# Kernel tuning notes

Measured on AMD Instinct MI355X. Metric: run time of the kernel, lower is better.

Reference implementation:

```python
import jax, jax.numpy as jnp
import numpy as np

H = 2048
MAX_DEPTH = 2
BASIS = 4


def setup_inputs() -> dict:
    key = jax.random.key(0)
    ks = jax.random.split(key, 16)
    s = 0.02

    def w(k, shape):
        return jax.random.normal(k, shape, dtype=jnp.float32) * s

    return dict(
        x=jax.random.normal(ks[0], (1, H), dtype=jnp.float32),
        h=jax.random.normal(ks[1], (1, H), dtype=jnp.float32),
        c=jax.random.normal(ks[2], (1, H), dtype=jnp.float32),
        Wq=w(ks[3], (H, H)), Wk=w(ks[4], (H, H)), Wv=w(ks[5], (H, H)), Wo=w(ks[6], (H, H)),
        Wih=w(ks[7], (H, 4 * H)), Whh=w(ks[8], (H, 4 * H)),
        b_lstm=jnp.zeros((4 * H,), jnp.float32),
        router_w=w(ks[9], (H, BASIS)), router_b=jnp.zeros((BASIS,), jnp.float32),
        expert_w=w(ks[10], (BASIS, H, H)), expert_b=jnp.zeros((BASIS, H), jnp.float32),
        dr_w=w(ks[11], (H, MAX_DEPTH + 1)),
        # bias the depth router toward the deepest choice so the recursion tree is exercised
        dr_b=jnp.array([0.0, 1.0, 5.0], jnp.float32),
        ram_w=w(ks[12], (2 * H, H)), ram_b=jnp.zeros((H,), jnp.float32),
        ag_w=w(ks[13], (2 * H, H)), ag_b=jnp.zeros((H,), jnp.float32),
    )


def reference(x, h, c, Wq, Wk, Wv, Wo, Wih, Whh, b_lstm, router_w, router_b,
              expert_w, expert_b, dr_w, dr_b, ram_w, ram_b, ag_w, ag_b):
    def cell_step(x_, h_, c_):
        # Single-token multi-head attention: softmax over a length-1 axis is
        # identically 1, so attention collapses to (h @ Wv) @ Wo; Wq/Wk are
        # parameters with zero effective gradient (matches torch behavior).
        attn = (h_ @ Wv) @ Wo
        gates = x_ @ Wih + attn @ Whh + b_lstm  # [1, 4H]
        i, f, g, o = jnp.split(gates, 4, axis=1)
        c2 = jax.nn.sigmoid(f) * c_ + jax.nn.sigmoid(i) * jnp.tanh(g)
        h2 = jax.nn.sigmoid(o) * jnp.tanh(c2)
        return h2, h2, c2

    def path_gate(hh):
        p = jax.nn.softmax(hh @ router_w + router_b, axis=1)          # [1, E]
        eo = jnp.einsum('bh,ehk->bek', hh, expert_w) + expert_b        # [1, E, H]
        return jnp.einsum('be,bek->bk', p, eo)                         # [1, H]

    def ramanujan(states):
        # alternating-harmonic (Ramanujan-summation style) weighted reduction
        agg = states[0] * 0.0
        for n, s in enumerate(states):
            agg = agg + (((-1.0) ** n) / (n + 1)) * s
        return jnp.concatenate([agg, states[0]], axis=1) @ ram_w + ram_b

    def fwd(x_, h_, c_, depth):
        so, hs, cs = cell_step(x_, h_, c_)
        hp = path_gate(hs)
        # mirrors torch.no_grad() + .item() host sync
        chosen = int(jnp.argmax(hp @ dr_w + dr_b, axis=1)[0])
        steps = min(chosen, max(0, MAX_DEPTH - depth))
        if steps <= 0:
            return so, hp, cs
        h_cur, c_cur, final = hp, cs, so
        states = [h_cur]
        for _ in range(steps):
            damping = 1.0 / (depth + 1) ** 2
            ro, hnr, cn = fwd(x_, h_cur, c_cur, depth + 1)
            h_next = h_cur + damping * (hnr - h_cur)  # torch.lerp
            states.append(h_next)
            h_cur, c_cur, final = h_next, cn, ro
        anchor = ramanujan(states)
        g = jax.nn.sigmoid(jnp.concatenate([h_cur, anchor], axis=1) @ ag_w + ag_b)
        return final, g * anchor + (1.0 - g) * h_cur, c_cur

    return fwd(x, h, c, 0)
```

## Files before the change

### kernel.cpp

```cpp
#include <hip/hip_runtime.h>
#include <math.h>


#define H 2048
#define NB 512
#define PREP_NB 2048
typedef unsigned short u16;
typedef float f4v __attribute__((ext_vector_type(4)));

struct P {
  const float *x, *h0, *c0, *Wv, *Wo, *Wih, *Whh, *b_lstm, *router_w, *router_b,
              *expert_w, *expert_b, *dr_w, *dr_b, *ram_w, *ram_b, *ag_w, *ag_b;
  const u16 *bWv, *bWo, *bWhh, *bEx, *bRam, *bAg;
  float* out;
  float* ws;
};

constexpr int CTRU   = 16384;
constexpr int DL     = 16384;
constexpr int GT     = 16400;
constexpr int NODE   = 24592;
constexpr int NODESZ = 26624;
constexpr int THV = 0, ATT = 2048, GAC = 4096, EO = 12288, SO = 20480, CS = 22528, HP = 24576;
constexpr int FIN    = NODE + 5 * NODESZ;
constexpr int FINSZ  = 8192;
constexpr int ANC = 0, GCC = 2048, HNo = 4096, AGGo = 6144;
constexpr int RH1 = FIN + 3 * FINSZ;
constexpr int RF1 = RH1 + 2048;
constexpr int RC1 = RH1 + 4096;
constexpr int ZTOT = 5 * 20480 + 3 * 4096;
constexpr size_t BF_BYTE_OFF = 786432;
constexpr size_t oWo  = 4194304;
constexpr size_t oWhh = 8388608;
constexpr size_t oEx  = 25165824;
constexpr size_t oRam = 41943040;
constexpr size_t oAg  = 50331648;
constexpr size_t BF_NODE = 41943040;
constexpr size_t BF_ALL  = 58720256;

__device__ __forceinline__ float sigm(float v) { return 1.f / (1.f + expf(-v)); }

__device__ __forceinline__ float coh_f(const float* p) {
  return __hip_atomic_load(p, __ATOMIC_RELAXED, __HIP_MEMORY_SCOPE_AGENT);
}
__device__ __forceinline__ void coh_st(float* p, float v) {
  __hip_atomic_store(p, v, __ATOMIC_RELAXED, __HIP_MEMORY_SCOPE_AGENT);
}

__device__ __forceinline__ float bfl(unsigned u) { union { unsigned x; float f; } c; c.x = u << 16; return c.f; }
__device__ __forceinline__ float bfh(unsigned u) { union { unsigned x; float f; } c; c.x = u & 0xFFFF0000u; return c.f; }
__device__ __forceinline__ u16 f2bf(float f) {
  unsigned u = __float_as_uint(f);
  u += 0x7FFFu + ((u >> 16) & 1u);
  return (u16)(u >> 16);
}

template <typename WT> struct W4;
template <> struct W4<float> {
  static __device__ __forceinline__ void load(const float* p, float* w) {
    const float4 v = *reinterpret_cast<const float4*>(p);
    w[0] = v.x; w[1] = v.y; w[2] = v.z; w[3] = v.w;
  }
};
template <> struct W4<u16> {
  static __device__ __forceinline__ void load(const u16* p, float* w) {
    const uint2 u = *reinterpret_cast<const uint2*>(p);
    w[0] = bfl(u.x); w[1] = bfh(u.x); w[2] = bfl(u.y); w[3] = bfh(u.y);
  }
};

template <typename WT> __device__ __forceinline__ const WT* selWv(const P& p);
template <> __device__ __forceinline__ const float* selWv<float>(const P& p) { return p.Wv; }
template <> __device__ __forceinline__ const u16*   selWv<u16>(const P& p)   { return p.bWv; }
template <typename WT> __device__ __forceinline__ const WT* selWo(const P& p);
template <> __device__ __forceinline__ const float* selWo<float>(const P& p) { return p.Wo; }
template <> __device__ __forceinline__ const u16*   selWo<u16>(const P& p)   { return p.bWo; }
template <typename WT> __device__ __forceinline__ const WT* selWhh(const P& p);
template <> __device__ __forceinline__ const float* selWhh<float>(const P& p) { return p.Whh; }
template <> __device__ __forceinline__ const u16*   selWhh<u16>(const P& p)   { return p.bWhh; }
template <typename WT> __device__ __forceinline__ const WT* selEx(const P& p);
template <> __device__ __forceinline__ const float* selEx<float>(const P& p) { return p.expert_w; }
template <> __device__ __forceinline__ const u16*   selEx<u16>(const P& p)   { return p.bEx; }
template <typename WT> __device__ __forceinline__ const WT* selRam(const P& p);
template <> __device__ __forceinline__ const float* selRam<float>(const P& p) { return p.ram_w; }
template <> __device__ __forceinline__ const u16*   selRam<u16>(const P& p)   { return p.bRam; }
template <typename WT> __device__ __forceinline__ const WT* selAg(const P& p);
template <> __device__ __forceinline__ const float* selAg<float>(const P& p) { return p.ag_w; }
template <> __device__ __forceinline__ const u16*   selAg<u16>(const P& p)   { return p.bAg; }

__device__ __forceinline__ int dsteps(const float* dla, const float* drb, int mx) {
  const float l0 = coh_f(dla + 0) + drb[0];
  const float l1 = coh_f(dla + 1) + drb[1];
  const float l2 = coh_f(dla + 2) + drb[2];
  int ch = 0; float bv = l0;
  if (l1 > bv) { bv = l1; ch = 1; }
  if (l2 > bv) { bv = l2; ch = 2; }
  return ch < mx ? ch : mx;
}

__device__ __forceinline__ bool pred(const float* ws, const float* drb, int code) {
  if (code == 0) return true;
  const int s0 = dsteps(ws + DL, drb, 2);
  switch (code) {
    case 1: return s0 >= 1;
    case 2: return s0 >= 1 && dsteps(ws + DL + 4, drb, 1) >= 1;
    case 3: return s0 >= 2;
    case 4: return s0 >= 2 && dsteps(ws + DL + 8, drb, 1) >= 1;
  }
  return true;
}

__device__ __forceinline__ void resbar(unsigned* ctr, int phase) {
  asm volatile("s_waitcnt vmcnt(0)" ::: "memory");
  __syncthreads();
  __shared__ int lastB;
  if (threadIdx.x == 0) {
    lastB = 0;
    unsigned* line = ctr + (blockIdx.x & 31) * 16;
    const unsigned prev = __hip_atomic_fetch_add(line, 1u, __ATOMIC_RELAXED, __HIP_MEMORY_SCOPE_AGENT);
    if (prev == (unsigned)(16 * phase) - 1u) {
      const unsigned m = __hip_atomic_fetch_add(ctr + 512, 1u, __ATOMIC_RELAXED, __HIP_MEMORY_SCOPE_AGENT);
      if (m == (unsigned)(32 * phase) - 1u) lastB = 1;
    }
  }
  __syncthreads();
  if (lastB) {
    if (threadIdx.x < 32)
      __hip_atomic_store(ctr + (40 + threadIdx.x) * 16, (unsigned)phase,
                         __ATOMIC_RELAXED, __HIP_MEMORY_SCOPE_AGENT);
  } else if (threadIdx.x == 0) {
    const unsigned* rel = ctr + (40 + (blockIdx.x & 31)) * 16;
    long t = 0;
    while (__hip_atomic_load(rel, __ATOMIC_RELAXED, __HIP_MEMORY_SCOPE_AGENT) < (unsigned)phase) {
      __builtin_amdgcn_s_sleep(2);
      if (++t > 30000000L) break;
    }
  }
  __syncthreads();
}

template <int CHUNK, int XMODE, typename WT>
__device__ __forceinline__ void gemv_phase(
    int bid, int G,
    const float* xA, const float* xB, int splitPt, const float* xBias,
    const WT* __restrict__ W, float* __restrict__ y, int N,
    float* shx, float4* red)
{
  const int tid = threadIdx.x, lane = tid & 63, tsub = tid >> 6;
  const int g = bid % G, s = bid / G;
  const int base = s * CHUNK;
  for (int idx = tid; idx < CHUNK; idx += 256) {
    const int i = base + idx;
    float v;
    if (XMODE == 0)      v = (i < splitPt) ? xA[i] : xB[i - splitPt];
    else if (XMODE == 1) v = coh_f(xA + i);
    else                 v = (i < splitPt) ? xA[i] : (xBias[i - splitPt] + coh_f(xB + (i - splitPt)));
    shx[idx] = v;
  }
  __syncthreads();
  constexpr int LEN = CHUNK / 4;
  const int j = (g << 8) + (lane << 2);
  const WT* Wp = W + (size_t)(base + tsub * LEN) * N + j;
  float ax = 0.f, ay = 0.f, az = 0.f, aw = 0.f;
#pragma unroll
  for (int t = 0; t < LEN; ++t) {
    const float xi = shx[tsub * LEN + t];
    float w[4];
    W4<WT>::load(Wp + (size_t)t * N, w);
    ax = fmaf(xi, w[0], ax); ay = fmaf(xi, w[1], ay);
    az = fmaf(xi, w[2], az); aw = fmaf(xi, w[3], aw);
  }
  red[tid] = make_float4(ax, ay, az, aw);
  __syncthreads();
  if (tsub == 0) {
    float4 a = red[tid], b = red[tid + 64], c = red[tid + 128], d = red[tid + 192];
    atomicAdd(&y[j + 0], a.x + b.x + c.x + d.x);
    atomicAdd(&y[j + 1], a.y + b.y + c.y + d.y);
    atomicAdd(&y[j + 2], a.z + b.z + c.z + d.z);
    atomicAdd(&y[j + 3], a.w + b.w + c.w + d.w);
  }
}

template <typename WT>
__device__ void expert_phase(const P& p, float* nb, const float* c_in, const float* gt,
                             float* shx, float4* red)
{
  const int tid = threadIdx.x, lane = tid & 63, w = tid >> 6;
  const int g = blockIdx.x & 31, s = blockIdx.x >> 5;
  const int i0 = s * 128;
  if (tid < 128) {
    const int i = i0 + tid;
    const float gi = p.b_lstm[i]         + coh_f(gt + i)         + coh_f(nb + GAC + i);
    const float gf = p.b_lstm[H + i]     + coh_f(gt + H + i)     + coh_f(nb + GAC + H + i);
    const float gg = p.b_lstm[2 * H + i] + coh_f(gt + 2 * H + i) + coh_f(nb + GAC + 2 * H + i);
    const float go = p.b_lstm[3 * H + i] + coh_f(gt + 3 * H + i) + coh_f(nb + GAC + 3 * H + i);
    const float c2 = sigm(gf) * c_in[i] + sigm(gi) * tanhf(gg);
    const float h2 = sigm(go) * tanhf(c2);
    shx[tid] = h2;
    if (g == 0) { coh_st(nb + SO + i, h2); coh_st(nb + CS + i, c2); }
  }
  __syncthreads();
  const int j = (g << 8) + (lane << 2);
  const int e = j >> 11, k = j & (H - 1);
  const WT* Wp = selEx<WT>(p) + ((size_t)e << 22) + (size_t)(i0 + w * 32) * H + k;
  float ax = 0.f, ay = 0.f, az = 0.f, aw = 0.f;
#pragma unroll
  for (int t = 0; t < 32; ++t) {
    const float xi = shx[w * 32 + t];
    float wv[4];
    W4<WT>::load(Wp + (size_t)t * H, wv);
    ax = fmaf(xi, wv[0], ax); ay = fmaf(xi, wv[1], ay);
    az = fmaf(xi, wv[2], az); aw = fmaf(xi, wv[3], aw);
  }
  red[tid] = make_float4(ax, ay, az, aw);
  __syncthreads();
  if (w == 0) {
    float4 a = red[tid], b = red[tid + 64], c = red[tid + 128], d = red[tid + 192];
    atomicAdd(&nb[EO + j + 0], a.x + b.x + c.x + d.x);
    atomicAdd(&nb[EO + j + 1], a.y + b.y + c.y + d.y);
    atomicAdd(&nb[EO + j + 2], a.z + b.z + c.z + d.z);
    atomicAdd(&nb[EO + j + 3], a.w + b.w + c.w + d.w);
  }
}

__device__ void combine_phase(const P& p, float* nb, float* dla, int leaf, float damping,
                              const float* php, float* hn, float* agg, float4* red)
{
  const int tid = threadIdx.x;
  float r0 = 0.f, r1 = 0.f, r2 = 0.f, r3 = 0.f;
  for (int i = tid; i < H; i += 256) {
    const float hh = coh_f(nb + SO + i);
    const float4 rw = *reinterpret_cast<const float4*>(p.router_w + i * 4);
    r0 = fmaf(hh, rw.x, r0); r1 = fmaf(hh, rw.y, r1);
    r2 = fmaf(hh, rw.z, r2); r3 = fmaf(hh, rw.w, r3);
  }
  red[tid] = make_float4(r0, r1, r2, r3);
  __syncthreads();
  for (int off = 128; off > 0; off >>= 1) {
    if (tid < off) {
      const float4 b = red[tid + off];
      red[tid].x += b.x; red[tid].y += b.y; red[tid].z += b.z; red[tid].w += b.w;
    }
    __syncthreads();
  }
  const float4 L = red[0];
  __syncthreads();
  const float l0 = L.x + p.router_b[0], l1 = L.y + p.router_b[1];
  const float l2 = L.z + p.router_b[2], l3 = L.w + p.router_b[3];
  const float m = fmaxf(fmaxf(l0, l1), fmaxf(l2, l3));
  const float e0 = expf(l0 - m), e1 = expf(l1 - m), e2 = expf(l2 - m), e3 = expf(l3 - m);
  const float inv = 1.f / (e0 + e1 + e2 + e3);
  const float q0 = e0 * inv, q1 = e1 * inv, q2 = e2 * inv, q3 = e3 * inv;
  const int jj = blockIdx.x * 256 + tid;
  const float v = q0 * (p.expert_b[jj]         + coh_f(nb + EO + jj))
                + q1 * (p.expert_b[H + jj]     + coh_f(nb + EO + H + jj))
                + q2 * (p.expert_b[2 * H + jj] + coh_f(nb + EO + 2 * H + jj))
                + q3 * (p.expert_b[3 * H + jj] + coh_f(nb + EO + 3 * H + jj));
  if (leaf) {
    const float h0v = php[jj];
    const float hnv = h0v + damping * (v - h0v);
    hn[jj] = hnv;
    agg[jj] = h0v - 0.5f * hnv;
  } else {
    nb[HP + jj] = v;
    red[tid] = make_float4(v * p.dr_w[jj * 3 + 0], v * p.dr_w[jj * 3 + 1], v * p.dr_w[jj * 3 + 2], 0.f);
    __syncthreads();
    for (int off = 128; off > 0; off >>= 1) {
      if (tid < off) {
        const float4 b = red[tid + off];
        red[tid].x += b.x; red[tid].y += b.y; red[tid].z += b.z;
      }
      __syncthreads();
    }
    if (tid == 0) {
      atomicAdd(&dla[0], red[0].x);
      atomicAdd(&dla[1], red[0].y);
      atomicAdd(&dla[2], red[0].z);
    }
  }
}

__device__ void tail_fsel(const P& p, float* ws) {
  if (dsteps(ws + DL, p.dr_b, 2) < 1) return;
  const bool deep = dsteps(ws + DL + 4, p.dr_b, 1) >= 1;
  const int jj = blockIdx.x * 256 + threadIdx.x;
  const float* n1 = ws + NODE + 1 * NODESZ;
  const float* n2 = ws + NODE + 2 * NODESZ;
  const float* fb = ws + FIN;
  float rh, rf, rc;
  if (deep) {
    const float gacc = p.ag_b[jj] + coh_f(fb + GCC + jj);
    const float anc  = p.ram_b[jj] + coh_f(fb + ANC + jj);
    const float g = sigm(gacc);
    rh = g * anc + (1.f - g) * fb[HNo + jj];
    rf = n2[SO + jj]; rc = n2[CS + jj];
  } else {
    rh = n1[HP + jj]; rf = n1[SO + jj]; rc = n1[CS + jj];
  }
  ws[RH1 + jj] = rh; ws[RF1 + jj] = rf; ws[RC1 + jj] = rc;
}

__device__ void tail1(const P& p, float* ws) {
  const int s0 = dsteps(ws + DL, p.dr_b, 2);
  if (s0 < 1) return;
  const int jj = blockIdx.x * 256 + threadIdx.x;
  const float* n0 = ws + NODE;
  const float* n3 = ws + NODE + 3 * NODESZ;
  const float* n4 = ws + NODE + 4 * NODESZ;
  const float* fb3 = ws + FIN + FINSZ;
  float* fb0 = ws + FIN + 2 * FINSZ;
  const float r1 = ws[RH1 + jj];
  float rh3 = 0.f, rf3 = 0.f, rc3 = 0.f;
  if (s0 >= 2) {
    if (dsteps(ws + DL + 8, p.dr_b, 1) >= 1) {
      const float gacc = p.ag_b[jj] + coh_f(fb3 + GCC + jj);
      const float anc  = p.ram_b[jj] + coh_f(fb3 + ANC + jj);
      const float g = sigm(gacc);
      rh3 = g * anc + (1.f - g) * fb3[HNo + jj];
      rf3 = n4[SO + jj]; rc3 = n4[CS + jj];
    } else { rh3 = n3[HP + jj]; rf3 = n3[SO + jj]; rc3 = n3[CS + jj]; }
  }
  float ag = n0[HP + jj] - 0.5f * r1;
  float hc, oF, oC;
  if (s0 >= 2) { ag += (1.f / 3.f) * rh3; hc = rh3; oF = rf3; oC = rc3; }
  else { hc = r1; oF = ws[RF1 + jj]; oC = ws[RC1 + jj]; }
  fb0[AGGo + jj] = ag; fb0[HNo + jj] = hc;
  p.out[jj] = oF; p.out[2 * H + jj] = oC;
}

__device__ void tail2(const P& p, float* ws) {
  const int s0 = dsteps(ws + DL, p.dr_b, 2);
  const int jj = blockIdx.x * 256 + threadIdx.x;
  const float* n0 = ws + NODE;
  const float* fb0 = ws + FIN + 2 * FINSZ;
  if (s0 == 0) {
    p.out[jj] = n0[SO + jj]; p.out[H + jj] = n0[HP + jj]; p.out[2 * H + jj] = n0[CS + jj];
  } else {
    const float gacc = p.ag_b[jj] + coh_f(fb0 + GCC + jj);
    const float anc  = p.ram_b[jj] + coh_f(fb0 + ANC + jj);
    const float g = sigm(gacc);
    p.out[H + jj] = g * anc + (1.f - g) * fb0[HNo + jj];
  }
}

__global__ void __launch_bounds__(256) k_zero(P p) {
  float* ws = p.ws;
  const int gtid = blockIdx.x * 256 + threadIdx.x;
  const int gsz = gridDim.x * 256;
  unsigned* u = (unsigned*)ws;
  for (int i = gtid; i < CTRU; i += gsz) u[i] = 0u;
  if (gtid < 12) ws[DL + gtid] = 0.f;
  for (int i = gtid; i < 8192; i += gsz) ws[GT + i] = 0.f;
}

__global__ void __launch_bounds__(256) k_prep(P p, u16* bf, int convMask) {
  float* ws = p.ws;
  __shared__ float shx[128];
  __shared__ float4 red[256];
  const size_t gtid = (size_t)blockIdx.x * 256 + threadIdx.x;
  const size_t nthr = (size_t)PREP_NB * 256;
  for (size_t i = gtid; i < (size_t)ZTOT; i += nthr) {
    if (i < 5 * 20480) {
      const int n = (int)(i / 20480), off = (int)(i % 20480);
      ws[NODE + n * NODESZ + off] = 0.f;
    } else {
      const int j = (int)(i - 5 * 20480);
      ws[FIN + (j >> 12) * FINSZ + (j & 4095)] = 0.f;
    }
  }
  auto conv = [&](const float* __restrict__ src, u16* __restrict__ dst, size_t elems) {
    for (size_t c = gtid; c < elems / 8; c += nthr) {
      const size_t e = c * 8;
      const f4v a = __builtin_nontemporal_load(reinterpret_cast<const f4v*>(src + e));
      const f4v b = __builtin_nontemporal_load(reinterpret_cast<const f4v*>(src + e + 4));
      uint4 o;
      o.x = (unsigned)f2bf(a.x) | ((unsigned)f2bf(a.y) << 16);
      o.y = (unsigned)f2bf(a.z) | ((unsigned)f2bf(a.w) << 16);
      o.z = (unsigned)f2bf(b.x) | ((unsigned)f2bf(b.y) << 16);
      o.w = (unsigned)f2bf(b.z) | ((unsigned)f2bf(b.w) << 16);
      *reinterpret_cast<uint4*>(dst + e) = o;
    }
  };
  if (convMask & 1) {
    conv(p.Wv,       bf,         oWo);
    conv(p.Wo,       bf + oWo,   oWhh - oWo);
    conv(p.Whh,      bf + oWhh,  oEx - oWhh);
    conv(p.expert_w, bf + oEx,   oRam - oEx);
  }
  if (convMask & 2) {
    conv(p.ram_w, bf + oRam, oAg - oRam);
    conv(p.ag_w,  bf + oAg,  BF_ALL - oAg);
  }
  gemv_phase<32, 0, float>(blockIdx.x, 32, p.x, p.x, 1 << 30, nullptr,
                           p.Wih, ws + GT, 4 * H, shx, red);
}

template <typename WT>
__global__ void __launch_bounds__(256, 2) k_node(
    P p, int nodeIdx, int ctrIdx, int predCode,
    const float* hv, const float* cv,
    int leaf, float damping, const float* php, float* hn, float* agg, float* dla)
{
  float* ws = p.ws;
  if (!pred(ws, p.dr_b, predCode)) return;
  __shared__ float shx[128];
  __shared__ float4 red[256];
  float* nb = ws + NODE + nodeIdx * NODESZ;
  unsigned* ctr = (unsigned*)ws + ctrIdx * 2048;
  gemv_phase<32, 0, WT>(blockIdx.x, 8, hv, hv, 1 << 30, nullptr, selWv<WT>(p), nb + THV, H, shx, red);
  resbar(ctr, 1);
  gemv_phase<32, 1, WT>(blockIdx.x, 8, nb + THV, nullptr, 0, nullptr, selWo<WT>(p), nb + ATT, H, shx, red);
  resbar(ctr, 2);
  gemv_phase<128, 1, WT>(blockIdx.x, 32, nb + ATT, nullptr, 0, nullptr, selWhh<WT>(p), nb + GAC, 4 * H, shx, red);
  resbar(ctr, 3);
  expert_phase<WT>(p, nb, cv, ws + GT, shx, red);
  resbar(ctr, 4);
  if (blockIdx.x >= 8) return;
  combine_phase(p, nb, dla, leaf, damping, php, hn, agg, red);
}

template <typename WT>
__global__ void __launch_bounds__(256, 2) k_fin(
    P p, int finIdx, int ctrIdx, int predCode,
    const float* aggv, const float* phpv, const float* hnv, int tailKind)
{
  float* ws = p.ws;
  __shared__ float shx[64];
  __shared__ float4 red[256];
  float* fb = ws + FIN + finIdx * FINSZ;
  unsigned* ctr = (unsigned*)ws + ctrIdx * 2048;
  const bool ok = pred(ws, p.dr_b, predCode);
  if (ok) {
    gemv_phase<64, 0, WT>(blockIdx.x, 8, aggv, phpv, H, nullptr, selRam<WT>(p), fb + ANC, H, shx, red);
    resbar(ctr, 1);
    gemv_phase<64, 2, WT>(blockIdx.x, 8, hnv, fb + ANC, H, p.ram_b, selAg<WT>(p), fb + GCC, H, shx, red);
    resbar(ctr, 2);
  }
  if (blockIdx.x >= 8) return;
  if (tailKind == 1) tail_fsel(p, ws);
  else if (tailKind == 2) tail1(p, ws);
  else tail2(p, ws);
}

extern "C" void kernel_launch(void* const* d_in, const int* in_sizes, int n_in,
                              void* d_out, int out_size, void* d_ws, size_t ws_size,
                              hipStream_t stream) {
  P p;
  p.x = (const float*)d_in[0];  p.h0 = (const float*)d_in[1];  p.c0 = (const float*)d_in[2];
  p.Wv = (const float*)d_in[5]; p.Wo = (const float*)d_in[6];
  p.Wih = (const float*)d_in[7]; p.Whh = (const float*)d_in[8];
  p.b_lstm = (const float*)d_in[9];
  p.router_w = (const float*)d_in[10]; p.router_b = (const float*)d_in[11];
  p.expert_w = (const float*)d_in[12]; p.expert_b = (const float*)d_in[13];
  p.dr_w = (const float*)d_in[14]; p.dr_b = (const float*)d_in[15];
  p.ram_w = (const float*)d_in[16]; p.ram_b = (const float*)d_in[17];
  p.ag_w = (const float*)d_in[18]; p.ag_b = (const float*)d_in[19];
  p.out = (float*)d_out;
  p.ws = (float*)d_ws;

  const bool useBf    = ws_size >= BF_BYTE_OFF + BF_NODE * 2 + 1024;
  const bool useBfFin = ws_size >= BF_BYTE_OFF + BF_ALL * 2 + 1024;
  u16* bf = (u16*)((char*)d_ws + BF_BYTE_OFF);
  p.bWv  = bf;        p.bWo = bf + oWo;  p.bWhh = bf + oWhh;
  p.bEx  = bf + oEx;  p.bRam = bf + oRam; p.bAg = bf + oAg;

  float* ws = p.ws;
  auto nb = [&](int n) { return ws + NODE + n * NODESZ; };
  float* fb1 = ws + FIN;
  float* fb3 = ws + FIN + FINSZ;
  float* fb0 = ws + FIN + 2 * FINSZ;

  auto node = [&](int n, int ctrIdx, int predCode, const float* hv, const float* cv,
                  int leaf, float damping, const float* php, float* hn, float* agg, float* dla) {
    if (useBf)
      k_node<u16><<<NB, 256, 0, stream>>>(p, n, ctrIdx, predCode, hv, cv, leaf, damping, php, hn, agg, dla);
    else
      k_node<float><<<NB, 256, 0, stream>>>(p, n, ctrIdx, predCode, hv, cv, leaf, damping, php, hn, agg, dla);
  };
  auto fin = [&](int f, int ctrIdx, int predCode, const float* aggv, const float* phpv,
                 const float* hnv, int tailKind) {
    if (useBfFin)
      k_fin<u16><<<NB, 256, 0, stream>>>(p, f, ctrIdx, predCode, aggv, phpv, hnv, tailKind);
    else
      k_fin<float><<<NB, 256, 0, stream>>>(p, f, ctrIdx, predCode, aggv, phpv, hnv, tailKind);
  };

  k_zero<<<16, 256, 0, stream>>>(p);
  k_prep<<<PREP_NB, 256, 0, stream>>>(p, bf, (useBf ? 1 : 0) | (useBfFin ? 2 : 0));
  node(0, 0, 0, p.h0, p.c0, 0, 0.f, nullptr, nullptr, nullptr, ws + DL);
  node(1, 1, 1, nb(0) + HP, nb(0) + CS, 0, 0.f, nullptr, nullptr, nullptr, ws + DL + 4);
  node(2, 2, 2, nb(1) + HP, nb(1) + CS, 1, 0.25f, nb(1) + HP, fb1 + HNo, fb1 + AGGo, nullptr);
  fin(0, 3, 2, fb1 + AGGo, nb(1) + HP, fb1 + HNo, 1);
  node(3, 4, 3, ws + RH1, ws + RC1, 0, 0.f, nullptr, nullptr, nullptr, ws + DL + 8);
  node(4, 5, 4, nb(3) + HP, nb(3) + CS, 1, 0.25f, nb(3) + HP, fb3 + HNo, fb3 + AGGo, nullptr);
  fin(1, 6, 4, fb3 + AGGo, nb(3) + HP, fb3 + HNo, 2);
  fin(2, 7, 1, fb0 + AGGo, nb(0) + HP, fb0 + HNo, 3);
}
```

Baseline: 356.2 us.

## Fuse bf16 weight conversion into first-use GEMV passes instead of a separate prep pass

Removes the standalone fp32-to-bf16 conversion from the prep kernel. The first node kernel and the first fin kernel now read fp32 weights, use them directly for their GEMVs, and write the bf16 copies as a side effect. Later nodes and fins read those bf16 copies. This is meant to save one full fp32 read of every weight matrix, since conversion and first use now share the same read. In exchange the first node becomes heavier, and the first fin must always run its GEMVs (ok || CONV) so that the bf16 ram/ag weights get written even when its predicate is false.

```diff
diff --git a/kernel.cpp b/kernel.cpp
--- a/kernel.cpp
+++ b/kernel.cpp
@@ -12,6 +12,7 @@
   const float *x, *h0, *c0, *Wv, *Wo, *Wih, *Whh, *b_lstm, *router_w, *router_b,
               *expert_w, *expert_b, *dr_w, *dr_b, *ram_w, *ram_b, *ag_w, *ag_b;
   const u16 *bWv, *bWo, *bWhh, *bEx, *bRam, *bAg;
+  u16 *mWv, *mWo, *mWhh, *mEx, *mRam, *mAg;
   float* out;
   float* ws;
 };
@@ -54,6 +55,9 @@
   u += 0x7FFFu + ((u >> 16) & 1u);
   return (u16)(u >> 16);
 }
+__device__ __forceinline__ unsigned pk2(float a, float b) {
+  return (unsigned)f2bf(a) | ((unsigned)f2bf(b) << 16);
+}
 
 template <typename WT> struct W4;
 template <> struct W4<float> {
@@ -139,12 +143,12 @@
   __syncthreads();
 }
 
-template <int CHUNK, int XMODE, typename WT>
+template <int CHUNK, int XMODE, typename WT, int CONV>
 __device__ __forceinline__ void gemv_phase(
     int bid, int G,
     const float* xA, const float* xB, int splitPt, const float* xBias,
     const WT* __restrict__ W, float* __restrict__ y, int N,
-    float* shx, float4* red)
+    u16* convDst, float* shx, float4* red)
 {
   const int tid = threadIdx.x, lane = tid & 63, tsub = tid >> 6;
   const int g = bid % G, s = bid / G;
@@ -166,7 +170,15 @@
   for (int t = 0; t < LEN; ++t) {
     const float xi = shx[tsub * LEN + t];
     float w[4];
-    W4<WT>::load(Wp + (size_t)t * N, w);
+    if constexpr (CONV) {
+      const f4v a = __builtin_nontemporal_load(
+          reinterpret_cast<const f4v*>(reinterpret_cast<const float*>(Wp) + (size_t)t * N));
+      w[0] = a.x; w[1] = a.y; w[2] = a.z; w[3] = a.w;
+      uint2 o; o.x = pk2(w[0], w[1]); o.y = pk2(w[2], w[3]);
+      *reinterpret_cast<uint2*>(convDst + (size_t)(base + tsub * LEN + t) * N + j) = o;
+    } else {
+      W4<WT>::load(Wp + (size_t)t * N, w);
+    }
     ax = fmaf(xi, w[0], ax); ay = fmaf(xi, w[1], ay);
     az = fmaf(xi, w[2], az); aw = fmaf(xi, w[3], aw);
   }
@@ -181,9 +193,9 @@
   }
 }
 
-template <typename WT>
+template <typename WT, int CONV>
 __device__ void expert_phase(const P& p, float* nb, const float* c_in, const float* gt,
-                             float* shx, float4* red)
+                             u16* convDst, float* shx, float4* red)
 {
   const int tid = threadIdx.x, lane = tid & 63, w = tid >> 6;
   const int g = blockIdx.x & 31, s = blockIdx.x >> 5;
@@ -202,13 +214,22 @@
   __syncthreads();
   const int j = (g << 8) + (lane << 2);
   const int e = j >> 11, k = j & (H - 1);
-  const WT* Wp = selEx<WT>(p) + ((size_t)e << 22) + (size_t)(i0 + w * 32) * H + k;
+  const size_t tileOff = ((size_t)e << 22) + (size_t)(i0 + w * 32) * H + k;
+  const WT* Wp = selEx<WT>(p) + tileOff;
   float ax = 0.f, ay = 0.f, az = 0.f, aw = 0.f;
 #pragma unroll
   for (int t = 0; t < 32; ++t) {
     const float xi = shx[w * 32 + t];
     float wv[4];
-    W4<WT>::load(Wp + (size_t)t * H, wv);
+    if constexpr (CONV) {
+      const f4v a = __builtin_nontemporal_load(
+          reinterpret_cast<const f4v*>(reinterpret_cast<const float*>(Wp) + (size_t)t * H));
+      wv[0] = a.x; wv[1] = a.y; wv[2] = a.z; wv[3] = a.w;
+      uint2 o; o.x = pk2(wv[0], wv[1]); o.y = pk2(wv[2], wv[3]);
+      *reinterpret_cast<uint2*>(convDst + tileOff + (size_t)t * H) = o;
+    } else {
+      W4<WT>::load(Wp + (size_t)t * H, wv);
+    }
     ax = fmaf(xi, wv[0], ax); ay = fmaf(xi, wv[1], ay);
     az = fmaf(xi, wv[2], az); aw = fmaf(xi, wv[3], aw);
   }
@@ -353,7 +374,7 @@
   for (int i = gtid; i < 8192; i += gsz) ws[GT + i] = 0.f;
 }
 
-__global__ void __launch_bounds__(256) k_prep(P p, u16* bf, int convMask) {
+__global__ void __launch_bounds__(256) k_prep(P p) {
   float* ws = p.ws;
   __shared__ float shx[128];
   __shared__ float4 red[256];
@@ -368,34 +389,11 @@
       ws[FIN + (j >> 12) * FINSZ + (j & 4095)] = 0.f;
     }
   }
-  auto conv = [&](const float* __restrict__ src, u16* __restrict__ dst, size_t elems) {
-    for (size_t c = gtid; c < elems / 8; c += nthr) {
-      const size_t e = c * 8;
-      const f4v a = __builtin_nontemporal_load(reinterpret_cast<const f4v*>(src + e));
-      const f4v b = __builtin_nontemporal_load(reinterpret_cast<const f4v*>(src + e + 4));
-      uint4 o;
-      o.x = (unsigned)f2bf(a.x) | ((unsigned)f2bf(a.y) << 16);
-      o.y = (unsigned)f2bf(a.z) | ((unsigned)f2bf(a.w) << 16);
-      o.z = (unsigned)f2bf(b.x) | ((unsigned)f2bf(b.y) << 16);
-      o.w = (unsigned)f2bf(b.z) | ((unsigned)f2bf(b.w) << 16);
-      *reinterpret_cast<uint4*>(dst + e) = o;
-    }
-  };
-  if (convMask & 1) {
-    conv(p.Wv,       bf,         oWo);
-    conv(p.Wo,       bf + oWo,   oWhh - oWo);
-    conv(p.Whh,      bf + oWhh,  oEx - oWhh);
-    conv(p.expert_w, bf + oEx,   oRam - oEx);
-  }
-  if (convMask & 2) {
-    conv(p.ram_w, bf + oRam, oAg - oRam);
-    conv(p.ag_w,  bf + oAg,  BF_ALL - oAg);
-  }
-  gemv_phase<32, 0, float>(blockIdx.x, 32, p.x, p.x, 1 << 30, nullptr,
-                           p.Wih, ws + GT, 4 * H, shx, red);
-}
-
-template <typename WT>
+  gemv_phase<32, 0, float, 0>(blockIdx.x, 32, p.x, p.x, 1 << 30, nullptr,
+                              p.Wih, ws + GT, 4 * H, nullptr, shx, red);
+}
+
+template <typename WT, int CONV>
 __global__ void __launch_bounds__(256, 2) k_node(
     P p, int nodeIdx, int ctrIdx, int predCode,
     const float* hv, const float* cv,
@@ -407,19 +405,22 @@
   __shared__ float4 red[256];
   float* nb = ws + NODE + nodeIdx * NODESZ;
   unsigned* ctr = (unsigned*)ws + ctrIdx * 2048;
-  gemv_phase<32, 0, WT>(blockIdx.x, 8, hv, hv, 1 << 30, nullptr, selWv<WT>(p), nb + THV, H, shx, red);
+  gemv_phase<32, 0, WT, CONV>(blockIdx.x, 8, hv, hv, 1 << 30, nullptr,
+                              selWv<WT>(p), nb + THV, H, p.mWv, shx, red);
   resbar(ctr, 1);
-  gemv_phase<32, 1, WT>(blockIdx.x, 8, nb + THV, nullptr, 0, nullptr, selWo<WT>(p), nb + ATT, H, shx, red);
+  gemv_phase<32, 1, WT, CONV>(blockIdx.x, 8, nb + THV, nullptr, 0, nullptr,
+                              selWo<WT>(p), nb + ATT, H, p.mWo, shx, red);
   resbar(ctr, 2);
-  gemv_phase<128, 1, WT>(blockIdx.x, 32, nb + ATT, nullptr, 0, nullptr, selWhh<WT>(p), nb + GAC, 4 * H, shx, red);
+  gemv_phase<128, 1, WT, CONV>(blockIdx.x, 32, nb + ATT, nullptr, 0, nullptr,
+                               selWhh<WT>(p), nb + GAC, 4 * H, p.mWhh, shx, red);
   resbar(ctr, 3);
-  expert_phase<WT>(p, nb, cv, ws + GT, shx, red);
+  expert_phase<WT, CONV>(p, nb, cv, ws + GT, p.mEx, shx, red);
   resbar(ctr, 4);
   if (blockIdx.x >= 8) return;
   combine_phase(p, nb, dla, leaf, damping, php, hn, agg, red);
 }
 
-template <typename WT>
+template <typename WT, int CONV>
 __global__ void __launch_bounds__(256, 2) k_fin(
     P p, int finIdx, int ctrIdx, int predCode,
     const float* aggv, const float* phpv, const float* hnv, int tailKind)
@@ -430,10 +431,12 @@
   float* fb = ws + FIN + finIdx * FINSZ;
   unsigned* ctr = (unsigned*)ws + ctrIdx * 2048;
   const bool ok = pred(ws, p.dr_b, predCode);
-  if (ok) {
-    gemv_phase<64, 0, WT>(blockIdx.x, 8, aggv, phpv, H, nullptr, selRam<WT>(p), fb + ANC, H, shx, red);
+  if (ok || CONV) {
+    gemv_phase<64, 0, WT, CONV>(blockIdx.x, 8, aggv, phpv, H, nullptr,
+                                selRam<WT>(p), fb + ANC, H, p.mRam, shx, red);
     resbar(ctr, 1);
-    gemv_phase<64, 2, WT>(blockIdx.x, 8, hnv, fb + ANC, H, p.ram_b, selAg<WT>(p), fb + GCC, H, shx, red);
+    gemv_phase<64, 2, WT, CONV>(blockIdx.x, 8, hnv, fb + ANC, H, p.ram_b,
+                                selAg<WT>(p), fb + GCC, H, p.mAg, shx, red);
     resbar(ctr, 2);
   }
   if (blockIdx.x >= 8) return;
@@ -461,8 +464,10 @@
   const bool useBf    = ws_size >= BF_BYTE_OFF + BF_NODE * 2 + 1024;
   const bool useBfFin = ws_size >= BF_BYTE_OFF + BF_ALL * 2 + 1024;
   u16* bf = (u16*)((char*)d_ws + BF_BYTE_OFF);
-  p.bWv  = bf;        p.bWo = bf + oWo;  p.bWhh = bf + oWhh;
-  p.bEx  = bf + oEx;  p.bRam = bf + oRam; p.bAg = bf + oAg;
+  p.bWv = bf;        p.bWo = bf + oWo;   p.bWhh = bf + oWhh;
+  p.bEx = bf + oEx;  p.bRam = bf + oRam; p.bAg  = bf + oAg;
+  p.mWv = bf;        p.mWo = bf + oWo;   p.mWhh = bf + oWhh;
+  p.mEx = bf + oEx;  p.mRam = bf + oRam; p.mAg  = bf + oAg;
 
   float* ws = p.ws;
   auto nb = [&](int n) { return ws + NODE + n * NODESZ; };
@@ -470,29 +475,38 @@
   float* fb3 = ws + FIN + FINSZ;
   float* fb0 = ws + FIN + 2 * FINSZ;
 
+  k_zero<<<16, 256, 0, stream>>>(p);
+  k_prep<<<PREP_NB, 256, 0, stream>>>(p);
+
+  if (useBf)
+    k_node<float, 1><<<NB, 256, 0, stream>>>(p, 0, 0, 0, p.h0, p.c0, 0, 0.f,
+                                             nullptr, nullptr, nullptr, ws + DL);
+  else
+    k_node<float, 0><<<NB, 256, 0, stream>>>(p, 0, 0, 0, p.h0, p.c0, 0, 0.f,
+                                             nullptr, nullptr, nullptr, ws + DL);
+
   auto node = [&](int n, int ctrIdx, int predCode, const float* hv, const float* cv,
                   int leaf, float damping, const float* php, float* hn, float* agg, float* dla) {
     if (useBf)
-      k_node<u16><<<NB, 256, 0, stream>>>(p, n, ctrIdx, predCode, hv, cv, leaf, damping, php, hn, agg, dla);
+      k_node<u16, 0><<<NB, 256, 0, stream>>>(p, n, ctrIdx, predCode, hv, cv, leaf, damping, php, hn, agg, dla);
     else
-      k_node<float><<<NB, 256, 0, stream>>>(p, n, ctrIdx, predCode, hv, cv, leaf, damping, php, hn, agg, dla);
+      k_node<float, 0><<<NB, 256, 0, stream>>>(p, n, ctrIdx, predCode, hv, cv, leaf, damping, php, hn, agg, dla);
   };
-  auto fin = [&](int f, int ctrIdx, int predCode, const float* aggv, const float* phpv,
-                 const float* hnv, int tailKind) {
-    if (useBfFin)
-      k_fin<u16><<<NB, 256, 0, stream>>>(p, f, ctrIdx, predCode, aggv, phpv, hnv, tailKind);
-    else
-      k_fin<float><<<NB, 256, 0, stream>>>(p, f, ctrIdx, predCode, aggv, phpv, hnv, tailKind);
-  };
-
-  k_zero<<<16, 256, 0, stream>>>(p);
-  k_prep<<<PREP_NB, 256, 0, stream>>>(p, bf, (useBf ? 1 : 0) | (useBfFin ? 2 : 0));
-  node(0, 0, 0, p.h0, p.c0, 0, 0.f, nullptr, nullptr, nullptr, ws + DL);
+
   node(1, 1, 1, nb(0) + HP, nb(0) + CS, 0, 0.f, nullptr, nullptr, nullptr, ws + DL + 4);
   node(2, 2, 2, nb(1) + HP, nb(1) + CS, 1, 0.25f, nb(1) + HP, fb1 + HNo, fb1 + AGGo, nullptr);
-  fin(0, 3, 2, fb1 + AGGo, nb(1) + HP, fb1 + HNo, 1);
+  if (useBfFin)
+    k_fin<float, 1><<<NB, 256, 0, stream>>>(p, 0, 3, 2, fb1 + AGGo, nb(1) + HP, fb1 + HNo, 1);
+  else
+    k_fin<float, 0><<<NB, 256, 0, stream>>>(p, 0, 3, 2, fb1 + AGGo, nb(1) + HP, fb1 + HNo, 1);
   node(3, 4, 3, ws + RH1, ws + RC1, 0, 0.f, nullptr, nullptr, nullptr, ws + DL + 8);
   node(4, 5, 4, nb(3) + HP, nb(3) + CS, 1, 0.25f, nb(3) + HP, fb3 + HNo, fb3 + AGGo, nullptr);
-  fin(1, 6, 4, fb3 + AGGo, nb(3) + HP, fb3 + HNo, 2);
-  fin(2, 7, 1, fb0 + AGGo, nb(0) + HP, fb0 + HNo, 3);
-}
+  if (useBfFin)
+    k_fin<u16, 0><<<NB, 256, 0, stream>>>(p, 1, 6, 4, fb3 + AGGo, nb(3) + HP, fb3 + HNo, 2);
+  else
+    k_fin<float, 0><<<NB, 256, 0, stream>>>(p, 1, 6, 4, fb3 + AGGo, nb(3) + HP, fb3 + HNo, 2);
+  if (useBfFin)
+    k_fin<u16, 0><<<NB, 256, 0, stream>>>(p, 2, 7, 1, fb0 + AGGo, nb(0) + HP, fb0 + HNo, 3);
+  else
+    k_fin<float, 0><<<NB, 256, 0, stream>>>(p, 2, 7, 1, fb0 + AGGo, nb(0) + HP, fb0 + HNo, 3);
+}
```

Result: faster. 345.7 us (-3.0%).
